# Optimization experiments

Hardware: AMD Instinct MI355X
Metric: run time of the kernel (lower is better)

The kernel has to match this reference:

```python
import jax, jax.numpy as jnp
import numpy as np
from jax import lax

H = 64  # LSTM units (hard-coded in the module)


def _lstm(x, W, U, b, return_sequences):
    """Keras-style LSTM (inference; recurrent_dropout inactive).
    x: [B, T, F]; W: [F, 4H]; U: [H, 4H]; b: [4H].
    Gate order (Keras): i, f, g(cell), o.
    """
    B = x.shape[0]
    # Precompute input contribution for all timesteps: [T, B, 4H]
    xz = jnp.einsum('btf,fg->tbg', x, W) + b

    def step(carry, z_t):
        h, c = carry
        z = z_t + h @ U  # [B, 4H]
        i = jax.nn.sigmoid(z[:, :H])
        f = jax.nn.sigmoid(z[:, H:2 * H])
        g = jnp.tanh(z[:, 2 * H:3 * H])
        o = jax.nn.sigmoid(z[:, 3 * H:])
        c = f * c + i * g
        h = o * jnp.tanh(c)
        return (h, c), h

    init = (jnp.zeros((B, H), x.dtype), jnp.zeros((B, H), x.dtype))
    (h_last, _), hs = lax.scan(step, init, xz)
    if return_sequences:
        return jnp.transpose(hs, (1, 0, 2))  # [B, T, H]
    return h_last  # [B, H]


def setup_inputs() -> dict:
    key = jax.random.key(0)
    ks = jax.random.split(key, 8)
    B, T, F = 4096, 256, 32
    s_in = 1.0 / np.sqrt(F)
    s_h = 1.0 / np.sqrt(H)
    return {
        'x': jax.random.normal(ks[0], (B, T, F), jnp.float32),
        'W1': jax.random.normal(ks[1], (F, 4 * H), jnp.float32) * s_in,
        'U1': jax.random.normal(ks[2], (H, 4 * H), jnp.float32) * s_h,
        'b1': jnp.zeros((4 * H,), jnp.float32),
        'W2': jax.random.normal(ks[3], (H, 4 * H), jnp.float32) * s_h,
        'U2': jax.random.normal(ks[4], (H, 4 * H), jnp.float32) * s_h,
        'b2': jnp.zeros((4 * H,), jnp.float32),
        'Wd': jax.random.normal(ks[5], (H, H), jnp.float32) * s_h,
        'bd': jnp.zeros((H,), jnp.float32),
        'Wo': jax.random.normal(ks[6], (H, 1), jnp.float32) * s_h,
        'bo': jnp.zeros((1,), jnp.float32),
    }


def reference(x, W1, U1, b1, W2, U2, b2, Wd, bd, Wo, bo):
    h_seq = _lstm(x, W1, U1, b1, return_sequences=True)   # hidden_lstm
    h_last = _lstm(h_seq, W2, U2, b2, return_sequences=False)  # lstm_layer
    d = jax.nn.sigmoid(h_last @ Wd + bd)  # Dense(64, sigmoid)
    return jax.nn.sigmoid(d @ Wo + bo)    # Dense(1, sigmoid) -> [B, 1]
```

## Files before the change

### kernel.cpp

```cpp
#include <hip/hip_runtime.h>
#include <hip/hip_bf16.h>


typedef __attribute__((ext_vector_type(8))) short short8;
typedef __attribute__((ext_vector_type(4))) float floatx4;
typedef __attribute__((ext_vector_type(2))) float floatx2;

__device__ __forceinline__ float ex2(float x){ return __builtin_amdgcn_exp2f(x); }
__device__ __forceinline__ float rcp_(float x){ return __builtin_amdgcn_rcpf(x); }
__device__ __forceinline__ float sigm(float x){ return rcp_(1.0f + ex2(-1.44269504f*x)); }
__device__ __forceinline__ unsigned bfbits(float f){
    unsigned u = __builtin_bit_cast(unsigned, f);
    u += 0x7FFFu + ((u >> 16) & 1u);
    return u >> 16;
}
__device__ __forceinline__ short f2bf(float f){ return (short)bfbits(f); }
__device__ __forceinline__ unsigned pack_bf2(float a, float b){
    float2 t; t.x = a; t.y = b;
    __hip_bfloat162 p = __float22bfloat162_rn(t);
    unsigned r; __builtin_memcpy(&r, &p, 4);
    return r;
}

#define MFMA_BF16 __builtin_amdgcn_mfma_f32_16x16x32_bf16

__device__ __forceinline__ float cellh(const floatx4& z, float& c){
    float iv = rcp_(1.0f + ex2(z[0]));
    float fv = rcp_(1.0f + ex2(z[1]));
    float rg = rcp_(1.0f + ex2(z[2]));
    float ov = rcp_(1.0f + ex2(z[3]));
    float gp = fmaf(-5.77078016f, rg, 2.88539008f);
    c = fmaf(fv, c, iv * gp);
    float th = fmaf(-2.0f, rcp_(1.0f + ex2(c)), 1.0f);
    return ov * th;
}

__global__ __launch_bounds__(1024, 1)
void lstm2_tz2(const float* __restrict__ x,
               const float* __restrict__ W1, const float* __restrict__ U1, const float* __restrict__ b1,
               const float* __restrict__ W2, const float* __restrict__ U2, const float* __restrict__ b2,
               const float* __restrict__ Wd, const float* __restrict__ bd,
               const float* __restrict__ Wo, const float* __restrict__ bo,
               float* __restrict__ out)
{
    __shared__ __align__(16) short h1s[2 * 1152];
    __shared__ __align__(16) short h2s[2 * 1152];
    __shared__ __align__(16) short xss[3 * 640];
    __shared__ float psum[4][16];

    const int tid  = threadIdx.x;
    const int w    = tid >> 6;
    const bool isL1 = (w < 8);
    const int wv   = isL1 ? w : (w - 8);
    const int lane = tid & 63;
    const int n    = lane & 15;
    const int q    = lane >> 4;
    const int b0   = blockIdx.x * 16;

    const float LG = 1.44269504f;

    const int ugl = n >> 2;
    const int gA  = n & 3;
    const float sA = (gA == 2) ? (2.0f * LG) : (-LG);

    short8  Wa[8];
    floatx4 bC[2];
    if (isL1) {
#pragma unroll
        for (int tt = 0; tt < 2; ++tt) {
            const int t = wv * 2 + tt;
            const int ncol = gA * 64 + t * 4 + ugl;
#pragma unroll
            for (int j = 0; j < 8; ++j) {
                const int k = q * 8 + j;
                Wa[tt * 3 + 0][j] = f2bf(W1[k * 256 + ncol] * sA);
                Wa[tt * 3 + 1][j] = f2bf(U1[k * 256 + ncol] * sA);
                Wa[tt * 3 + 2][j] = f2bf(U1[(32 + k) * 256 + ncol] * sA);
            }
#pragma unroll
            for (int r = 0; r < 4; ++r)
                bC[tt][r] = b1[r * 64 + t * 4 + q] * ((r == 2) ? (2.0f * LG) : (-LG));
        }
    } else {
#pragma unroll
        for (int tt = 0; tt < 2; ++tt) {
            const int t = wv * 2 + tt;
            const int ncol = gA * 64 + t * 4 + ugl;
#pragma unroll
            for (int j = 0; j < 8; ++j) {
                const int k = q * 8 + j;
                Wa[tt * 4 + 0][j] = f2bf(W2[k * 256 + ncol] * sA);
                Wa[tt * 4 + 1][j] = f2bf(W2[(32 + k) * 256 + ncol] * sA);
                Wa[tt * 4 + 2][j] = f2bf(U2[k * 256 + ncol] * sA);
                Wa[tt * 4 + 3][j] = f2bf(U2[(32 + k) * 256 + ncol] * sA);
            }
#pragma unroll
            for (int r = 0; r < 4; ++r)
                bC[tt][r] = b2[r * 64 + t * 4 + q] * ((r == 2) ? (2.0f * LG) : (-LG));
        }
    }

    {
        unsigned* p1 = (unsigned*)&h1s[0];
        unsigned* p2 = (unsigned*)&h2s[0];
        for (int i = tid; i < 1152; i += 1024) { p1[i] = 0u; p2[i] = 0u; }
    }

    const int srow = wv * 2 + q;
    const int scol = (lane & 15) * 2;
    const float* xp = x + (size_t)(b0 + srow) * 8192 + scol;
    const bool stager = isL1 && (lane < 32);
    floatx2 xv0;
    if (stager) {
        floatx2 v0 = *(const floatx2*)xp;
        floatx2 v1 = *(const floatx2*)(xp + 32);
        *(unsigned*)&xss[0   + srow * 40 + scol] = pack_bf2(v0.x, v0.y);
        *(unsigned*)&xss[640 + srow * 40 + scol] = pack_bf2(v1.x, v1.y);
        xv0 = *(const floatx2*)(xp + 64);
    }
    __syncthreads();

    const int rdA = n * 72 + q * 8;
    const int rdB = rdA + 32;
    const int rdX = n * 40 + q * 8;

    float c[2] = {0, 0};
    int xb0 = 0, xb1 = 1, xb2 = 2;

    short8 bx_cur;
    if (isL1) bx_cur = *(const short8*)&xss[rdX];

    for (int u = 0; u <= 256; ++u) {
        const int par = u & 1, pax = par ^ 1;
        if (isL1) {
            if (u < 256) {
                short8 h1a = *(const short8*)&h1s[pax * 1152 + rdA];
                short8 h1c = *(const short8*)&h1s[pax * 1152 + rdB];
#pragma unroll
                for (int tt = 0; tt < 2; ++tt) {
                    floatx4 z = bC[tt];
                    z = MFMA_BF16(Wa[tt * 3 + 0], bx_cur, z, 0, 0, 0);
                    z = MFMA_BF16(Wa[tt * 3 + 1], h1a,    z, 0, 0, 0);
                    z = MFMA_BF16(Wa[tt * 3 + 2], h1c,    z, 0, 0, 0);
                    float hv = cellh(z, c[tt]);
                    float hp = __shfl_xor(hv, 16, 64);
                    if (!(q & 1))
                        *(unsigned*)&h1s[par * 1152 + n * 72 + (wv * 2 + tt) * 4 + q]
                            = pack_bf2(hv, hp);
                }
                if (stager && u < 254) {
                    *(unsigned*)&xss[xb2 * 640 + srow * 40 + scol] = pack_bf2(xv0.x, xv0.y);
                    if (u < 253) xv0 = *(const floatx2*)(xp + (size_t)(u + 3) * 32);
                }
                if (u < 255) bx_cur = *(const short8*)&xss[xb1 * 640 + rdX];
            }
        } else {
            if (u >= 1) {
                short8 bh0 = *(const short8*)&h1s[pax * 1152 + rdA];
                short8 bh1 = *(const short8*)&h1s[pax * 1152 + rdB];
                short8 bg0 = *(const short8*)&h2s[par * 1152 + rdA];
                short8 bg1 = *(const short8*)&h2s[par * 1152 + rdB];
#pragma unroll
                for (int tt = 0; tt < 2; ++tt) {
                    floatx4 z = bC[tt];
                    z = MFMA_BF16(Wa[tt * 4 + 0], bh0, z, 0, 0, 0);
                    z = MFMA_BF16(Wa[tt * 4 + 1], bh1, z, 0, 0, 0);
                    z = MFMA_BF16(Wa[tt * 4 + 2], bg0, z, 0, 0, 0);
                    z = MFMA_BF16(Wa[tt * 4 + 3], bg1, z, 0, 0, 0);
                    float hv = cellh(z, c[tt]);
                    float hp = __shfl_xor(hv, 16, 64);
                    if (!(q & 1))
                        *(unsigned*)&h2s[pax * 1152 + n * 72 + (wv * 2 + tt) * 4 + q]
                            = pack_bf2(hv, hp);
                }
            }
        }
        { int t0 = xb0; xb0 = xb1; xb1 = xb2; xb2 = t0; }
        __syncthreads();
    }

    if (!isL1 && wv < 4) {
        const int colD = wv * 16 + n;
        short8 wd0, wd1;
#pragma unroll
        for (int j = 0; j < 8; ++j) {
            wd0[j] = f2bf(Wd[(q * 8 + j) * 64 + colD] * (-LG));
            wd1[j] = f2bf(Wd[(32 + q * 8 + j) * 64 + colD] * (-LG));
        }
        short8 hA0 = *(const short8*)&h2s[1152 + rdA];
        short8 hA1 = *(const short8*)&h2s[1152 + rdB];
        const float bdv = bd[colD] * (-LG);
        floatx4 dacc = { bdv, bdv, bdv, bdv };
        dacc = MFMA_BF16(hA0, wd0, dacc, 0, 0, 0);
        dacc = MFMA_BF16(hA1, wd1, dacc, 0, 0, 0);
        const float wo = Wo[colD];
#pragma unroll
        for (int r = 0; r < 4; ++r) {
            float p = rcp_(1.0f + ex2(dacc[r])) * wo;
            p += __shfl_xor(p, 1, 64);
            p += __shfl_xor(p, 2, 64);
            p += __shfl_xor(p, 4, 64);
            p += __shfl_xor(p, 8, 64);
            if (n == 0) psum[wv][q * 4 + r] = p;
        }
    }
    __syncthreads();
    if (tid < 16) {
        float s = psum[0][tid] + psum[1][tid] + psum[2][tid] + psum[3][tid] + bo[0];
        out[b0 + tid] = sigm(s);
    }
}

extern "C" void kernel_launch(void* const* d_in, const int* in_sizes, int n_in,
                              void* d_out, int out_size, void* d_ws, size_t ws_size,
                              hipStream_t stream) {
    (void)in_sizes; (void)n_in; (void)d_ws; (void)ws_size; (void)out_size;
    const float* x  = (const float*)d_in[0];
    const float* W1 = (const float*)d_in[1];
    const float* U1 = (const float*)d_in[2];
    const float* b1 = (const float*)d_in[3];
    const float* W2 = (const float*)d_in[4];
    const float* U2 = (const float*)d_in[5];
    const float* b2 = (const float*)d_in[6];
    const float* Wd = (const float*)d_in[7];
    const float* bd = (const float*)d_in[8];
    const float* Wo = (const float*)d_in[9];
    const float* bo = (const float*)d_in[10];
    lstm2_tz2<<<dim3(256), dim3(1024), 0, stream>>>(
        x, W1, U1, b1, W2, U2, b2, Wd, bd, Wo, bo, (float*)d_out);
}
```

Measured before the change: 388.0 us.

## Load x directly into MFMA registers, merge gate reciprocals, drop shuffle stores

Removes the shared-memory staging ring for x. Each layer-1 lane now loads its own 8 floats per step straight from global memory into registers, one step ahead, and converts them to a bf16 operand. The cell math is reworked to share reciprocals (i*g and o*tanh(c) each use one rcp of a product), with c clamped so ex2 stays finite. The cross-lane shuffle and packed 32-bit stores are replaced by 16-bit stores of each h value. The aim is fewer LDS operations, shuffles and transcendental calls on the serial recurrence path, at the cost of per-step global load latency sitting close to the critical path and more narrow LDS writes.

```diff
diff --git a/kernel.cpp b/kernel.cpp
--- a/kernel.cpp
+++ b/kernel.cpp
@@ -4,7 +4,7 @@
 
 typedef __attribute__((ext_vector_type(8))) short short8;
 typedef __attribute__((ext_vector_type(4))) float floatx4;
-typedef __attribute__((ext_vector_type(2))) float floatx2;
+typedef __attribute__((ext_vector_type(4))) int   intx4;
 
 __device__ __forceinline__ float ex2(float x){ return __builtin_amdgcn_exp2f(x); }
 __device__ __forceinline__ float rcp_(float x){ return __builtin_amdgcn_rcpf(x); }
@@ -21,22 +21,34 @@
     unsigned r; __builtin_memcpy(&r, &p, 4);
     return r;
 }
+__device__ __forceinline__ short8 cvt8(const floatx4& a, const floatx4& b){
+    intx4 p;
+    p[0] = (int)pack_bf2(a[0], a[1]);
+    p[1] = (int)pack_bf2(a[2], a[3]);
+    p[2] = (int)pack_bf2(b[0], b[1]);
+    p[3] = (int)pack_bf2(b[2], b[3]);
+    return __builtin_bit_cast(short8, p);
+}
 
 #define MFMA_BF16 __builtin_amdgcn_mfma_f32_16x16x32_bf16
 
 __device__ __forceinline__ float cellh(const floatx4& z, float& c){
-    float iv = rcp_(1.0f + ex2(z[0]));
-    float fv = rcp_(1.0f + ex2(z[1]));
-    float rg = rcp_(1.0f + ex2(z[2]));
-    float ov = rcp_(1.0f + ex2(z[3]));
-    float gp = fmaf(-5.77078016f, rg, 2.88539008f);
-    c = fmaf(fv, c, iv * gp);
-    float th = fmaf(-2.0f, rcp_(1.0f + ex2(c)), 1.0f);
-    return ov * th;
+    float e0 = ex2(z[0]);
+    float e1 = ex2(z[1]);
+    float e2 = ex2(z[2]);
+    float e3 = ex2(z[3]);
+    float fr = rcp_(1.0f + e1);
+    float pr = rcp_((1.0f + e0) * (1.0f + e2));
+    float ig = (e2 - 1.0f) * pr;
+    c = fmaf(fr, c, 2.88539008f * ig);
+    c = fminf(fmaxf(c, -80.0f), 80.0f);
+    float ec = ex2(c);
+    float hr = rcp_((1.0f + e3) * (1.0f + ec));
+    return (ec - 1.0f) * hr;
 }
 
 __global__ __launch_bounds__(1024, 1)
-void lstm2_tz2(const float* __restrict__ x,
+void lstm2_tz3(const float* __restrict__ x,
                const float* __restrict__ W1, const float* __restrict__ U1, const float* __restrict__ b1,
                const float* __restrict__ W2, const float* __restrict__ U2, const float* __restrict__ b2,
                const float* __restrict__ Wd, const float* __restrict__ bd,
@@ -45,7 +57,6 @@
 {
     __shared__ __align__(16) short h1s[2 * 1152];
     __shared__ __align__(16) short h2s[2 * 1152];
-    __shared__ __align__(16) short xss[3 * 640];
     __shared__ float psum[4][16];
 
     const int tid  = threadIdx.x;
@@ -106,29 +117,24 @@
         for (int i = tid; i < 1152; i += 1024) { p1[i] = 0u; p2[i] = 0u; }
     }
 
-    const int srow = wv * 2 + q;
-    const int scol = (lane & 15) * 2;
-    const float* xp = x + (size_t)(b0 + srow) * 8192 + scol;
-    const bool stager = isL1 && (lane < 32);
-    floatx2 xv0;
-    if (stager) {
-        floatx2 v0 = *(const floatx2*)xp;
-        floatx2 v1 = *(const floatx2*)(xp + 32);
-        *(unsigned*)&xss[0   + srow * 40 + scol] = pack_bf2(v0.x, v0.y);
-        *(unsigned*)&xss[640 + srow * 40 + scol] = pack_bf2(v1.x, v1.y);
-        xv0 = *(const floatx2*)(xp + 64);
+    const float* xlane = x + (size_t)(b0 + n) * 8192 + q * 8;
+    floatx4 xlo, xhi;
+    short8  bx;
+    if (isL1) {
+        xlo = *(const floatx4*)(xlane);
+        xhi = *(const floatx4*)(xlane + 4);
     }
     __syncthreads();
+    if (isL1) {
+        bx  = cvt8(xlo, xhi);
+        xlo = *(const floatx4*)(xlane + 32);
+        xhi = *(const floatx4*)(xlane + 36);
+    }
 
     const int rdA = n * 72 + q * 8;
     const int rdB = rdA + 32;
-    const int rdX = n * 40 + q * 8;
 
     float c[2] = {0, 0};
-    int xb0 = 0, xb1 = 1, xb2 = 2;
-
-    short8 bx_cur;
-    if (isL1) bx_cur = *(const short8*)&xss[rdX];
 
     for (int u = 0; u <= 256; ++u) {
         const int par = u & 1, pax = par ^ 1;
@@ -139,20 +145,19 @@
 #pragma unroll
                 for (int tt = 0; tt < 2; ++tt) {
                     floatx4 z = bC[tt];
-                    z = MFMA_BF16(Wa[tt * 3 + 0], bx_cur, z, 0, 0, 0);
-                    z = MFMA_BF16(Wa[tt * 3 + 1], h1a,    z, 0, 0, 0);
-                    z = MFMA_BF16(Wa[tt * 3 + 2], h1c,    z, 0, 0, 0);
+                    z = MFMA_BF16(Wa[tt * 3 + 0], bx,  z, 0, 0, 0);
+                    z = MFMA_BF16(Wa[tt * 3 + 1], h1a, z, 0, 0, 0);
+                    z = MFMA_BF16(Wa[tt * 3 + 2], h1c, z, 0, 0, 0);
                     float hv = cellh(z, c[tt]);
-                    float hp = __shfl_xor(hv, 16, 64);
-                    if (!(q & 1))
-                        *(unsigned*)&h1s[par * 1152 + n * 72 + (wv * 2 + tt) * 4 + q]
-                            = pack_bf2(hv, hp);
+                    h1s[par * 1152 + n * 72 + (wv * 2 + tt) * 4 + q] = f2bf(hv);
                 }
-                if (stager && u < 254) {
-                    *(unsigned*)&xss[xb2 * 640 + srow * 40 + scol] = pack_bf2(xv0.x, xv0.y);
-                    if (u < 253) xv0 = *(const floatx2*)(xp + (size_t)(u + 3) * 32);
+                if (u < 255) {
+                    bx = cvt8(xlo, xhi);
+                    if (u < 254) {
+                        xlo = *(const floatx4*)(xlane + (size_t)(u + 2) * 32);
+                        xhi = *(const floatx4*)(xlane + (size_t)(u + 2) * 32 + 4);
+                    }
                 }
-                if (u < 255) bx_cur = *(const short8*)&xss[xb1 * 640 + rdX];
             }
         } else {
             if (u >= 1) {
@@ -168,14 +173,10 @@
                     z = MFMA_BF16(Wa[tt * 4 + 2], bg0, z, 0, 0, 0);
                     z = MFMA_BF16(Wa[tt * 4 + 3], bg1, z, 0, 0, 0);
                     float hv = cellh(z, c[tt]);
-                    float hp = __shfl_xor(hv, 16, 64);
-                    if (!(q & 1))
-                        *(unsigned*)&h2s[pax * 1152 + n * 72 + (wv * 2 + tt) * 4 + q]
-                            = pack_bf2(hv, hp);
+                    h2s[pax * 1152 + n * 72 + (wv * 2 + tt) * 4 + q] = f2bf(hv);
                 }
             }
         }
-        { int t0 = xb0; xb0 = xb1; xb1 = xb2; xb2 = t0; }
         __syncthreads();
     }
 
@@ -226,6 +227,6 @@
     const float* bd = (const float*)d_in[8];
     const float* Wo = (const float*)d_in[9];
     const float* bo = (const float*)d_in[10];
-    lstm2_tz2<<<dim3(256), dim3(1024), 0, stream>>>(
+    lstm2_tz3<<<dim3(256), dim3(1024), 0, stream>>>(
         x, W1, U1, b1, W2, U2, b2, Wd, bd, Wo, bo, (float*)d_out);
 }
```

Result: slower. 502.4 us (+29.5%).
